# Optimization experiments

Hardware: AMD Instinct MI355X
Metric: run time of the kernel (lower is better)

Reference implementation:

```python
import jax, jax.numpy as jnp
import numpy as np

EMBED_DIM = 1024


def setup_inputs() -> dict:
    key = jax.random.key(0)
    ks = jax.random.split(key, 9)
    B, S, D = 4, 4096, EMBED_DIM
    s = 1.0 / np.sqrt(D)
    inp = {"x": jax.random.normal(ks[0], (B, S, D), dtype=jnp.float32)}
    names = ["q", "k", "v", "out"]
    for i, n in enumerate(names):
        inp[f"w_{n}"] = jax.random.uniform(ks[1 + 2 * i], (D, D), jnp.float32, -s, s)
        inp[f"b_{n}"] = jax.random.uniform(ks[2 + 2 * i], (D,), jnp.float32, -s, s)
    return inp


def reference(x, w_q, b_q, w_k, b_k, w_v, b_v, w_out, b_out):
    D = x.shape[-1]
    scaling = 1.0 / jnp.sqrt(jnp.asarray(D, x.dtype))
    q = jnp.einsum("bsd,ed->bse", x, w_q) + b_q
    k = jnp.einsum("bsd,ed->bse", x, w_k) + b_k
    v = jnp.einsum("bsd,ed->bse", x, w_v) + b_v
    # full [B, S, S] attention matrix, as in the original module
    scores = jnp.einsum("bqd,bkd->bqk", q, k) * scaling
    attn = jax.nn.softmax(scores, axis=-1)
    out = jnp.einsum("bqk,bkd->bqd", attn, v)
    return jnp.einsum("bsd,ed->bse", out, w_out) + b_out
```

## Files before the change

kernel.cpp:

```cpp
#include <hip/hip_runtime.h>
#include <hip/hip_bf16.h>

typedef __hip_bfloat16 bf16;
typedef __bf16 bf16x8 __attribute__((ext_vector_type(8)));
typedef float f32x4 __attribute__((ext_vector_type(4)));

#define B_ 4
#define S_ 4096
#define D_ 1024
#define BS_ 16384
#define N3_ 3072

__device__ __forceinline__ void gld_lds16(const void* g, void* l) {
    __builtin_amdgcn_global_load_lds(
        (const __attribute__((address_space(1))) void*)g,
        (__attribute__((address_space(3))) void*)l, 16, 0, 0);
}

__device__ __forceinline__ void cast4_one(const float* __restrict__ in,
                                          bf16* __restrict__ out, int i) {
    float4 v = ((const float4*)in)[i];
    union { ushort4 u; bf16 h[4]; } cv;
    cv.h[0] = __float2bfloat16(v.x);
    cv.h[1] = __float2bfloat16(v.y);
    cv.h[2] = __float2bfloat16(v.z);
    cv.h[3] = __float2bfloat16(v.w);
    ((ushort4*)out)[i] = cv.u;
}

__global__ __launch_bounds__(256) void prologue(
    const float* __restrict__ x, const float* __restrict__ wq,
    const float* __restrict__ wk, const float* __restrict__ wv,
    const float* __restrict__ wo, const float* __restrict__ bq,
    const float* __restrict__ bk, const float* __restrict__ bv,
    bf16* __restrict__ xb, bf16* __restrict__ Wc, bf16* __restrict__ Wo,
    float* __restrict__ bc, float* __restrict__ ls) {
    const int blk = blockIdx.x, tid = threadIdx.x;
    if (blk < 16384) {
        cast4_one(x, xb, blk * 256 + tid);
    } else if (blk < 20480) {
        int w = (blk - 16384) >> 10;
        int i = ((blk - 16384) & 1023) * 256 + tid;
        const float* src = (w == 0) ? wq : (w == 1) ? wk : (w == 2) ? wv : wo;
        bf16* dst = (w == 3) ? Wo : Wc + (long)w * D_ * D_;
        cast4_one(src, dst, i);
    } else if (blk < 20544) {
        ls[(blk - 20480) * 256 + tid] = 0.f;
    } else {
        for (int i = tid; i < N3_; i += 256)
            bc[i] = (i < 1024) ? bq[i] : (i < 2048) ? bk[i - 1024] : bv[i - 2048];
    }
}

__global__ __launch_bounds__(256) void transpose_v(const bf16* __restrict__ QKV,
                                                   bf16* __restrict__ VT) {
    __shared__ bf16 t[32][33];
    const int b = blockIdx.z;
    const bf16* Vb = QKV + (long)b * S_ * N3_ + 2048;
    bf16* VTb = VT + (long)b * D_ * S_;
    const int s0 = blockIdx.x * 32, d0 = blockIdx.y * 32;
    const int r = threadIdx.x >> 5, c = threadIdx.x & 31;
#pragma unroll
    for (int i = 0; i < 4; i++)
        t[r + i * 8][c] = Vb[(long)(s0 + r + i * 8) * N3_ + d0 + c];
    __syncthreads();
#pragma unroll
    for (int i = 0; i < 4; i++)
        VTb[(long)(d0 + r + i * 8) * S_ + s0 + c] = t[c][r + i * 8];
}

template <int EPI>
__global__ __launch_bounds__(256, 2) void gemm_nt(
    const bf16* __restrict__ A, int lda, long sA,
    const bf16* __restrict__ B, int ldb, long sB,
    void* __restrict__ Cout, int ldc, long sC,
    int K, const float* __restrict__ bias,
    float* __restrict__ rowsum, int sL, float scale) {
    __shared__ __align__(16) bf16 As[128 * 32];
    __shared__ __align__(16) bf16 Bs[128 * 32];
    const int tid = threadIdx.x;
    const int lane = tid & 63;
    const int wave = tid >> 6;
    const int bz = blockIdx.z;
    const int m0 = blockIdx.x * 128, n0 = blockIdx.y * 128;
    A += (long)bz * sA;
    B += (long)bz * sB;
    rowsum += (long)bz * sL;

    const int wr = (wave >> 1) * 64;
    const int wc = (wave & 1) * 64;
    const int fm = lane & 15;
    const int q4 = lane >> 4;
    const int rdoff = ((q4 ^ ((fm >> 1) & 3)) << 3);

    const int c0 = tid, c1 = tid + 256;
    const int r0 = c0 >> 2, q0 = (((c0 & 3) ^ ((c0 >> 3) & 3)) << 3);
    const int r1 = c1 >> 2, q1 = (((c1 & 3) ^ ((c1 >> 3) & 3)) << 3);

    f32x4 zero = {0.f, 0.f, 0.f, 0.f};
    f32x4 acc[4][4];
#pragma unroll
    for (int i = 0; i < 4; i++)
#pragma unroll
        for (int j = 0; j < 4; j++) acc[i][j] = zero;

    for (int k0 = 0; k0 < K; k0 += 32) {
        gld_lds16(A + (long)(m0 + r0) * lda + k0 + q0, As + c0 * 8);
        gld_lds16(A + (long)(m0 + r1) * lda + k0 + q1, As + c1 * 8);
        gld_lds16(B + (long)(n0 + r0) * ldb + k0 + q0, Bs + c0 * 8);
        gld_lds16(B + (long)(n0 + r1) * ldb + k0 + q1, Bs + c1 * 8);
        __syncthreads();
        bf16x8 af[4], bfr[4];
#pragma unroll
        for (int i = 0; i < 4; i++) {
            af[i]  = *(const bf16x8*)(As + (wr + i * 16 + fm) * 32 + rdoff);
            bfr[i] = *(const bf16x8*)(Bs + (wc + i * 16 + fm) * 32 + rdoff);
        }
#pragma unroll
        for (int i = 0; i < 4; i++)
#pragma unroll
            for (int j = 0; j < 4; j++)
                acc[i][j] = __builtin_amdgcn_mfma_f32_16x16x32_bf16(
                    af[i], bfr[j], acc[i][j], 0, 0, 0);
        __syncthreads();
    }

#pragma unroll
    for (int i = 0; i < 4; i++)
#pragma unroll
        for (int r = 0; r < 4; r++) {
            const int grow = m0 + wr + q4 * 4 + i * 16 + r;
            if constexpr (EPI == 0) {
#pragma unroll
                for (int j = 0; j < 4; j++) {
                    int gcol = n0 + wc + j * 16 + fm;
                    ((bf16*)Cout)[(long)bz * sC + (long)grow * ldc + gcol] =
                        __float2bfloat16(acc[i][j][r] + bias[gcol]);
                }
            } else if constexpr (EPI == 1) {
                float s = 0.f;
#pragma unroll
                for (int j = 0; j < 4; j++) {
                    int gcol = n0 + wc + j * 16 + fm;
                    float v = __expf(acc[i][j][r] * scale);
                    bf16 hv = __float2bfloat16(v);
                    ((bf16*)Cout)[(long)bz * sC + (long)grow * ldc + gcol] = hv;
                    s += __bfloat162float(hv);
                }
                s += __shfl_xor(s, 1, 16);
                s += __shfl_xor(s, 2, 16);
                s += __shfl_xor(s, 4, 16);
                s += __shfl_xor(s, 8, 16);
                if (fm == 0) atomicAdd(rowsum + grow, s);
            } else if constexpr (EPI == 2) {
                float inv = 1.0f / rowsum[grow];
#pragma unroll
                for (int j = 0; j < 4; j++) {
                    int gcol = n0 + wc + j * 16 + fm;
                    ((bf16*)Cout)[(long)bz * sC + (long)grow * ldc + gcol] =
                        __float2bfloat16(acc[i][j][r] * inv);
                }
            } else {
#pragma unroll
                for (int j = 0; j < 4; j++) {
                    int gcol = n0 + wc + j * 16 + fm;
                    ((float*)Cout)[(long)bz * sC + (long)grow * ldc + gcol] =
                        acc[i][j][r] + bias[gcol];
                }
            }
        }
}

extern "C" void kernel_launch(void* const* d_in, const int* in_sizes, int n_in,
                              void* d_out, int out_size, void* d_ws, size_t ws_size,
                              hipStream_t stream) {
    const float* x  = (const float*)d_in[0];
    const float* wq = (const float*)d_in[1];
    const float* bq = (const float*)d_in[2];
    const float* wk = (const float*)d_in[3];
    const float* bk = (const float*)d_in[4];
    const float* wv = (const float*)d_in[5];
    const float* bv = (const float*)d_in[6];
    const float* wo = (const float*)d_in[7];
    const float* bo = (const float*)d_in[8];
    (void)in_sizes; (void)n_in; (void)out_size;

    char* p = (char*)d_ws;
    bf16* Wc  = (bf16*)p;  p += (long)N3_ * D_ * 2;
    bf16* Wo  = (bf16*)p;  p += (long)D_ * D_ * 2;
    float* bc = (float*)p; p += N3_ * 4;
    bf16* QKV = (bf16*)p;  p += (long)BS_ * N3_ * 2;
    float* ls = (float*)p; p += (long)BS_ * 4;
    const bool big = ws_size >= 142684160UL;
    bf16* VT = big ? (bf16*)p : (bf16*)((char*)d_out + 33554432);

    bf16* xb = (bf16*)d_out;
    bf16* E  = (bf16*)d_out;

    prologue<<<dim3(20545), 256, 0, stream>>>(x, wq, wk, wv, wo, bq, bk, bv,
                                              xb, Wc, Wo, bc, ls);

    gemm_nt<0><<<dim3(BS_ / 128, N3_ / 128, 1), 256, 0, stream>>>(
        xb, D_, 0, Wc, D_, 0, QKV, N3_, 0, D_, bc, ls, 0, 1.f);

    transpose_v<<<dim3(S_ / 32, D_ / 32, B_), 256, 0, stream>>>(QKV, VT);

    if (big) {
        for (int pr = 0; pr < 2; ++pr) {
            const long qoff = (long)(2 * pr) * S_ * N3_;
            gemm_nt<1><<<dim3(32, 32, 2), 256, 0, stream>>>(
                QKV + qoff, N3_, (long)S_ * N3_,
                QKV + qoff + 1024, N3_, (long)S_ * N3_,
                E, S_, (long)S_ * S_,
                D_, nullptr, ls + 2 * pr * S_, S_, 0.03125f);
            gemm_nt<2><<<dim3(32, 8, 2), 256, 0, stream>>>(
                E, S_, (long)S_ * S_,
                VT + (long)(2 * pr) * D_ * S_, S_, (long)D_ * S_,
                QKV + qoff, N3_, (long)S_ * N3_,
                S_, nullptr, ls + 2 * pr * S_, S_, 1.f);
        }
    } else {
        for (int b = 0; b < B_; ++b) {
            const long qoff = (long)b * S_ * N3_;
            gemm_nt<1><<<dim3(32, 32, 1), 256, 0, stream>>>(
                QKV + qoff, N3_, 0, QKV + qoff + 1024, N3_, 0,
                E, S_, 0, D_, nullptr, ls + b * S_, 0, 0.03125f);
            gemm_nt<2><<<dim3(32, 8, 1), 256, 0, stream>>>(
                E, S_, 0, VT + (long)b * D_ * S_, S_, 0,
                QKV + qoff, N3_, 0, S_, nullptr, ls + b * S_, 0, 1.f);
        }
    }

    gemm_nt<3><<<dim3(BS_ / 128, D_ / 128, 1), 256, 0, stream>>>(
        QKV, N3_, 0, Wo, D_, 0, d_out, D_, 0, D_, bo, ls, 0, 1.f);
}
```

Measured before the change: 677.8 us.

## Double K-tile depth to 64, template M-tile, and drop batched-pair attention path

The GEMM kernel now loads 64-wide K slices per iteration, using a new 8-chunk XOR swizzle, which halves the number of barrier pairs per K. It is also templated on the M tile size so the PV GEMM can run 64-row tiles with twice as many blocks (64x8 grid), giving better occupancy on the narrow N=1024 output. The two-batches-per-launch path that depended on workspace size is removed, so all attention runs per batch with VT placed in the output buffer. LDS use doubles to 32KB per block, which may limit residency, and the per-batch loop may give up the concurrency the batched path had when the workspace was large.

Result: faster. 650.3 us (-4.1%).

```diff
diff --git a/kernel.cpp b/kernel.cpp
--- a/kernel.cpp
+++ b/kernel.cpp
@@ -69,64 +69,78 @@
         VTb[(long)(d0 + r + i * 8) * S_ + s0 + c] = t[c][r + i * 8];
 }
 
-template <int EPI>
+template <int EPI, int BM>
 __global__ __launch_bounds__(256, 2) void gemm_nt(
     const bf16* __restrict__ A, int lda, long sA,
     const bf16* __restrict__ B, int ldb, long sB,
     void* __restrict__ Cout, int ldc, long sC,
     int K, const float* __restrict__ bias,
     float* __restrict__ rowsum, int sL, float scale) {
-    __shared__ __align__(16) bf16 As[128 * 32];
-    __shared__ __align__(16) bf16 Bs[128 * 32];
+    constexpr int MI = BM / 32;
+    __shared__ __align__(16) bf16 As[BM * 64];
+    __shared__ __align__(16) bf16 Bs[128 * 64];
     const int tid = threadIdx.x;
     const int lane = tid & 63;
     const int wave = tid >> 6;
     const int bz = blockIdx.z;
-    const int m0 = blockIdx.x * 128, n0 = blockIdx.y * 128;
+    const int m0 = blockIdx.x * BM, n0 = blockIdx.y * 128;
     A += (long)bz * sA;
     B += (long)bz * sB;
     rowsum += (long)bz * sL;
 
-    const int wr = (wave >> 1) * 64;
+    const int wr = (wave >> 1) * (BM / 2);
     const int wc = (wave & 1) * 64;
     const int fm = lane & 15;
     const int q4 = lane >> 4;
-    const int rdoff = ((q4 ^ ((fm >> 1) & 3)) << 3);
-
-    const int c0 = tid, c1 = tid + 256;
-    const int r0 = c0 >> 2, q0 = (((c0 & 3) ^ ((c0 >> 3) & 3)) << 3);
-    const int r1 = c1 >> 2, q1 = (((c1 & 3) ^ ((c1 >> 3) & 3)) << 3);
+    const int sw = fm & 7;
+    const int rd0 = ((q4 ^ sw) << 3);
+    const int rd1 = (((4 + q4) ^ sw) << 3);
 
     f32x4 zero = {0.f, 0.f, 0.f, 0.f};
-    f32x4 acc[4][4];
-#pragma unroll
-    for (int i = 0; i < 4; i++)
+    f32x4 acc[MI][4];
+#pragma unroll
+    for (int i = 0; i < MI; i++)
 #pragma unroll
         for (int j = 0; j < 4; j++) acc[i][j] = zero;
 
-    for (int k0 = 0; k0 < K; k0 += 32) {
-        gld_lds16(A + (long)(m0 + r0) * lda + k0 + q0, As + c0 * 8);
-        gld_lds16(A + (long)(m0 + r1) * lda + k0 + q1, As + c1 * 8);
-        gld_lds16(B + (long)(n0 + r0) * ldb + k0 + q0, Bs + c0 * 8);
-        gld_lds16(B + (long)(n0 + r1) * ldb + k0 + q1, Bs + c1 * 8);
+    for (int k0 = 0; k0 < K; k0 += 64) {
+#pragma unroll
+        for (int t = 0; t < BM / 32; t++) {
+            int c = tid + t * 256;
+            int row = c >> 3;
+            int q = (((c & 7) ^ (row & 7)) << 3);
+            gld_lds16(A + (long)(m0 + row) * lda + k0 + q, As + c * 8);
+        }
+#pragma unroll
+        for (int t = 0; t < 4; t++) {
+            int c = tid + t * 256;
+            int row = c >> 3;
+            int q = (((c & 7) ^ (row & 7)) << 3);
+            gld_lds16(B + (long)(n0 + row) * ldb + k0 + q, Bs + c * 8);
+        }
         __syncthreads();
-        bf16x8 af[4], bfr[4];
-#pragma unroll
-        for (int i = 0; i < 4; i++) {
-            af[i]  = *(const bf16x8*)(As + (wr + i * 16 + fm) * 32 + rdoff);
-            bfr[i] = *(const bf16x8*)(Bs + (wc + i * 16 + fm) * 32 + rdoff);
-        }
-#pragma unroll
-        for (int i = 0; i < 4; i++)
+#pragma unroll
+        for (int kh = 0; kh < 2; kh++) {
+            const int rdo = kh ? rd1 : rd0;
+            bf16x8 af[MI], bfr[4];
+#pragma unroll
+            for (int i = 0; i < MI; i++)
+                af[i] = *(const bf16x8*)(As + (wr + i * 16 + fm) * 64 + rdo);
 #pragma unroll
             for (int j = 0; j < 4; j++)
-                acc[i][j] = __builtin_amdgcn_mfma_f32_16x16x32_bf16(
-                    af[i], bfr[j], acc[i][j], 0, 0, 0);
+                bfr[j] = *(const bf16x8*)(Bs + (wc + j * 16 + fm) * 64 + rdo);
+#pragma unroll
+            for (int i = 0; i < MI; i++)
+#pragma unroll
+                for (int j = 0; j < 4; j++)
+                    acc[i][j] = __builtin_amdgcn_mfma_f32_16x16x32_bf16(
+                        af[i], bfr[j], acc[i][j], 0, 0, 0);
+        }
         __syncthreads();
     }
 
 #pragma unroll
-    for (int i = 0; i < 4; i++)
+    for (int i = 0; i < MI; i++)
 #pragma unroll
         for (int r = 0; r < 4; r++) {
             const int grow = m0 + wr + q4 * 4 + i * 16 + r;
@@ -183,7 +197,7 @@
     const float* bv = (const float*)d_in[6];
     const float* wo = (const float*)d_in[7];
     const float* bo = (const float*)d_in[8];
-    (void)in_sizes; (void)n_in; (void)out_size;
+    (void)in_sizes; (void)n_in; (void)out_size; (void)ws_size;
 
     char* p = (char*)d_ws;
     bf16* Wc  = (bf16*)p;  p += (long)N3_ * D_ * 2;
@@ -191,46 +205,29 @@
     float* bc = (float*)p; p += N3_ * 4;
     bf16* QKV = (bf16*)p;  p += (long)BS_ * N3_ * 2;
     float* ls = (float*)p; p += (long)BS_ * 4;
-    const bool big = ws_size >= 142684160UL;
-    bf16* VT = big ? (bf16*)p : (bf16*)((char*)d_out + 33554432);
 
     bf16* xb = (bf16*)d_out;
+    bf16* VT = (bf16*)((char*)d_out + 33554432);
     bf16* E  = (bf16*)d_out;
 
     prologue<<<dim3(20545), 256, 0, stream>>>(x, wq, wk, wv, wo, bq, bk, bv,
                                               xb, Wc, Wo, bc, ls);
 
-    gemm_nt<0><<<dim3(BS_ / 128, N3_ / 128, 1), 256, 0, stream>>>(
+    gemm_nt<0, 128><<<dim3(BS_ / 128, N3_ / 128, 1), 256, 0, stream>>>(
         xb, D_, 0, Wc, D_, 0, QKV, N3_, 0, D_, bc, ls, 0, 1.f);
 
     transpose_v<<<dim3(S_ / 32, D_ / 32, B_), 256, 0, stream>>>(QKV, VT);
 
-    if (big) {
-        for (int pr = 0; pr < 2; ++pr) {
-            const long qoff = (long)(2 * pr) * S_ * N3_;
-            gemm_nt<1><<<dim3(32, 32, 2), 256, 0, stream>>>(
-                QKV + qoff, N3_, (long)S_ * N3_,
-                QKV + qoff + 1024, N3_, (long)S_ * N3_,
-                E, S_, (long)S_ * S_,
-                D_, nullptr, ls + 2 * pr * S_, S_, 0.03125f);
-            gemm_nt<2><<<dim3(32, 8, 2), 256, 0, stream>>>(
-                E, S_, (long)S_ * S_,
-                VT + (long)(2 * pr) * D_ * S_, S_, (long)D_ * S_,
-                QKV + qoff, N3_, (long)S_ * N3_,
-                S_, nullptr, ls + 2 * pr * S_, S_, 1.f);
-        }
-    } else {
-        for (int b = 0; b < B_; ++b) {
-            const long qoff = (long)b * S_ * N3_;
-            gemm_nt<1><<<dim3(32, 32, 1), 256, 0, stream>>>(
-                QKV + qoff, N3_, 0, QKV + qoff + 1024, N3_, 0,
-                E, S_, 0, D_, nullptr, ls + b * S_, 0, 0.03125f);
-            gemm_nt<2><<<dim3(32, 8, 1), 256, 0, stream>>>(
-                E, S_, 0, VT + (long)b * D_ * S_, S_, 0,
-                QKV + qoff, N3_, 0, S_, nullptr, ls + b * S_, 0, 1.f);
-        }
+    for (int b = 0; b < B_; ++b) {
+        const long qoff = (long)b * S_ * N3_;
+        gemm_nt<1, 128><<<dim3(32, 32, 1), 256, 0, stream>>>(
+            QKV + qoff, N3_, 0, QKV + qoff + 1024, N3_, 0,
+            E, S_, 0, D_, nullptr, ls + b * S_, 0, 0.03125f);
+        gemm_nt<2, 64><<<dim3(64, 8, 1), 256, 0, stream>>>(
+            E, S_, 0, VT + (long)b * D_ * S_, S_, 0,
+            QKV + qoff, N3_, 0, S_, nullptr, ls + b * S_, 0, 1.f);
     }
 
-    gemm_nt<3><<<dim3(BS_ / 128, D_ / 128, 1), 256, 0, stream>>>(
+    gemm_nt<3, 128><<<dim3(BS_ / 128, D_ / 128, 1), 256, 0, stream>>>(
         QKV, N3_, 0, Wo, D_, 0, d_out, D_, 0, D_, bo, ls, 0, 1.f);
 }
```
